# Performance work log

Measured on AMD Instinct MI355X. Metric: run time of the kernel, lower is better.

Reference implementation:

```python
import jax, jax.numpy as jnp
import numpy as np

PAD, BOS, EOS = 0, 1, 2
VOCAB, EMB, HID, BATCH, MAXLEN = 32, 64, 1024, 2048, 100


def setup_inputs() -> dict:
    key = jax.random.key(0)
    ks = jax.random.split(key, 11)
    s = 0.08  # small init scale keeps softmax/sigmoid in a sane range
    g = lambda k, shape: (s * jax.random.normal(k, shape)).astype(jnp.float32)
    emb = g(ks[0], (VOCAB, EMB)).at[PAD].set(0.0)  # padding_idx row = 0
    return {
        "prevs": jnp.full((BATCH, 1), BOS, dtype=jnp.int32),
        "emb": emb,
        "Wih0": g(ks[1], (4 * HID, EMB)),
        "Whh0": g(ks[2], (4 * HID, HID)),
        "bih0": g(ks[3], (4 * HID,)),
        "bhh0": g(ks[4], (4 * HID,)),
        "Wih1": g(ks[5], (4 * HID, HID)),
        "Whh1": g(ks[6], (4 * HID, HID)),
        "bih1": g(ks[7], (4 * HID,)),
        "bhh1": g(ks[8], (4 * HID,)),
        "Wout": g(ks[9], (VOCAB, HID)),
        "bout": g(ks[10], (VOCAB,)),
        "max_len": MAXLEN,
    }


def _lstm_cell(x, h, c, Wih, Whh, bih, bhh):
    # torch LSTM gate order: i, f, g, o
    gates = x @ Wih.T + bih + h @ Whh.T + bhh  # [n, 4H]
    i, f, g, o = jnp.split(gates, 4, axis=-1)
    c = jax.nn.sigmoid(f) * c + jax.nn.sigmoid(i) * jnp.tanh(g)
    h = jax.nn.sigmoid(o) * jnp.tanh(c)
    return h, c


def reference(prevs, emb, Wih0, Whh0, bih0, bhh0, Wih1, Whh1, bih1, bhh1,
              Wout, bout, max_len):
    n = prevs.shape[0]
    H = Whh0.shape[1]
    prev = prevs[:, 0].astype(jnp.int32)
    h0 = jnp.zeros((n, H), jnp.float32)
    c0 = jnp.zeros((n, H), jnp.float32)
    h1 = jnp.zeros((n, H), jnp.float32)
    c1 = jnp.zeros((n, H), jnp.float32)
    is_end = prev == EOS
    lengths = jnp.zeros((n,), jnp.int32)
    keys = jax.random.split(jax.random.key(42), max_len)

    def step(carry, k):
        prev, h0, c0, h1, c1, is_end, lengths = carry
        x = emb[prev]                                   # [n, E]
        h0, c0 = _lstm_cell(x, h0, c0, Wih0, Whh0, bih0, bhh0)
        h1, c1 = _lstm_cell(h0, h1, c1, Wih1, Whh1, bih1, bhh1)
        logits = h1 @ Wout.T + bout                     # [n, V]
        cur = jax.random.categorical(k, logits).astype(jnp.int32)
        cur = jnp.where(is_end, PAD, cur)               # finished rows emit PAD
        lengths = lengths + (~is_end).astype(jnp.int32)
        is_end = is_end | (cur == EOS)
        return (cur, h0, c0, h1, c1, is_end, lengths), cur

    carry, seq = jax.lax.scan(step, (prev, h0, c0, h1, c1, is_end, lengths), keys)
    lengths = carry[6] + 1                               # +1 for BOS, as in sample_tensor
    sequences = jnp.concatenate([prevs.astype(jnp.int32), seq.T], axis=1)  # [n, 1+max_len]
    return sequences, lengths
```

## Files before the change

kernel.cpp:

```cpp
#include <hip/hip_runtime.h>
#include <cstdint>
#include <cstddef>


constexpr int PAD_TOK = 0, BOS_TOK = 1, EOS_TOK = 2;
constexpr int VOCAB = 32, EMB = 64, HID = 1024, BATCH = 2048, MAXLEN = 100;
constexpr int BK = 32;
constexpr int NKT_H = HID / BK;
constexpr float SCALE = 64.0f;
constexpr double INV_S2 = 1.0 / 4096.0;

using half8 = __attribute__((ext_vector_type(8))) _Float16;
using f32x4 = __attribute__((ext_vector_type(4))) float;
typedef unsigned short u16;
typedef uint32_t u32;

__device__ __forceinline__ u32 rotl32(u32 v, int d) {
  return (v << d) | (v >> (32 - d));
}

__device__ __forceinline__ void threefry2x32(u32 k0, u32 k1, u32 x0, u32 x1,
                                             u32& y0, u32& y1) {
  const u32 k2 = k0 ^ k1 ^ 0x1BD11BDAu;
#define TF_ROUND(r) do { x0 += x1; x1 = rotl32(x1, (r)); x1 ^= x0; } while (0)
  x0 += k0; x1 += k1;
  TF_ROUND(13); TF_ROUND(15); TF_ROUND(26); TF_ROUND(6);
  x0 += k1; x1 += k2 + 1u;
  TF_ROUND(17); TF_ROUND(29); TF_ROUND(16); TF_ROUND(24);
  x0 += k2; x1 += k0 + 2u;
  TF_ROUND(13); TF_ROUND(15); TF_ROUND(26); TF_ROUND(6);
  x0 += k0; x1 += k1 + 3u;
  TF_ROUND(17); TF_ROUND(29); TF_ROUND(16); TF_ROUND(24);
  x0 += k1; x1 += k2 + 4u;
  TF_ROUND(13); TF_ROUND(15); TF_ROUND(26); TF_ROUND(6);
  x0 += k2; x1 += k0 + 5u;
#undef TF_ROUND
  y0 = x0; y1 = x1;
}

__device__ __forceinline__ void gl_lds16(const void* g, void* l) {
  __builtin_amdgcn_global_load_lds(
      (const __attribute__((address_space(1))) void*)g,
      (__attribute__((address_space(3))) void*)l, 16, 0, 0);
}

__device__ __forceinline__ double rcp1p(double q) {
  const double d = 1.0 + q;
  double r = (double)__builtin_amdgcn_rcpf((float)d);
  r = r * fma(-d, r, 2.0);
  r = r * fma(-d, r, 2.0);
  return r;
}
__device__ __forceinline__ double exp2d(double t) {
  const double n = rint(t);
  const double f = t - n;
  double p = 1.0178086009239699e-07;
  p = fma(p, f, 1.3215542443841225e-06);
  p = fma(p, f, 1.5252733804059840e-05);
  p = fma(p, f, 1.5403530393381610e-04);
  p = fma(p, f, 1.3333558146428443e-03);
  p = fma(p, f, 9.6181291076284772e-03);
  p = fma(p, f, 5.5504108664821580e-02);
  p = fma(p, f, 2.4022650695910071e-01);
  p = fma(p, f, 6.9314718055994531e-01);
  p = fma(p, f, 1.0);
  const long long e = ((long long)(int)n + 1023) << 52;
  return p * __longlong_as_double(e);
}
__device__ __forceinline__ double sigd(double x) {
  return rcp1p(exp2d(x * -1.4426950408889634));
}
__device__ __forceinline__ double tanhd(double x) {
  return fma(2.0, rcp1p(exp2d(x * -2.8853900817779268)), -1.0);
}

__global__ __launch_bounds__(256) void pack_w(
    const float* __restrict__ src, int K, int nkt,
    uint4* __restrict__ dhi, uint4* __restrict__ dlo, int nchunks) {
  const int g = blockIdx.x * 256 + threadIdx.x;
  if (g >= nchunks) return;
  const int ut = g / (nkt * 512);
  const int rem = g - ut * (nkt * 512);
  const int kt = rem >> 9;
  const int slot = rem & 511;
  const int fm = slot >> 6, kg = (slot >> 4) & 3, r15 = slot & 15;
  const int row = (fm & 3) * HID + ut * 32 + (fm >> 2) * 16 + r15;
  const int col = kt * 32 + kg * 8;
  const float* s = src + (size_t)row * K + col;
  u16 hh[8], ll[8];
#pragma unroll
  for (int e = 0; e < 8; ++e) {
    const float x = s[e] * SCALE;
    const _Float16 h = (_Float16)x;
    const float rm = x - (float)h;
    const _Float16 l = (_Float16)rm;
    hh[e] = __builtin_bit_cast(u16, h);
    ll[e] = __builtin_bit_cast(u16, l);
  }
  dhi[g] = make_uint4((u32)hh[0] | ((u32)hh[1] << 16),
                      (u32)hh[2] | ((u32)hh[3] << 16),
                      (u32)hh[4] | ((u32)hh[5] << 16),
                      (u32)hh[6] | ((u32)hh[7] << 16));
  dlo[g] = make_uint4((u32)ll[0] | ((u32)ll[1] << 16),
                      (u32)ll[2] | ((u32)ll[3] << 16),
                      (u32)ll[4] | ((u32)ll[5] << 16),
                      (u32)ll[6] | ((u32)ll[7] << 16));
}

__global__ __launch_bounds__(256) void split_kernel(
    const float* __restrict__ src, u16* __restrict__ hi, u16* __restrict__ lo,
    int n) {
  const int i = blockIdx.x * 256 + threadIdx.x;
  if (i >= n) return;
  const float x = src[i] * SCALE;
  const _Float16 h = (_Float16)x;
  const float rem = x - (float)h;
  const _Float16 l = (_Float16)rem;
  hi[i] = __builtin_bit_cast(u16, h);
  lo[i] = __builtin_bit_cast(u16, l);
}

__global__ __launch_bounds__(256) void init_kernel(
    const int* __restrict__ prevs, float* __restrict__ c0,
    float* __restrict__ c1, u16* __restrict__ h0hi0, u16* __restrict__ h0lo0,
    u16* __restrict__ h0hi1, u16* __restrict__ h0lo1,
    u16* __restrict__ h1hi0, u16* __restrict__ h1lo0,
    u16* __restrict__ h1hi1, u16* __restrict__ h1lo1,
    int* __restrict__ prev, int* __restrict__ is_end,
    int* __restrict__ lengths, u32* __restrict__ keys,
    int* __restrict__ out_tok) {
  const int tid = blockIdx.x * 256 + threadIdx.x;
  const int total = BATCH * HID;
  if (tid < total) {
    c0[tid] = 0.0f; c1[tid] = 0.0f;
    h0hi0[tid] = 0; h0lo0[tid] = 0; h0hi1[tid] = 0; h0lo1[tid] = 0;
    h1hi0[tid] = 0; h1lo0[tid] = 0; h1hi1[tid] = 0; h1lo1[tid] = 0;
  }
  if (tid < BATCH) {
    const int p = prevs[tid];
    prev[tid] = p;
    is_end[tid] = (p == EOS_TOK) ? 1 : 0;
    lengths[tid] = 0;
    out_tok[(size_t)tid * (MAXLEN + 1)] = p;
  }
  if (tid < MAXLEN) {
    u32 y0, y1;
    threefry2x32(0u, 42u, 0u, (u32)tid, y0, y1);
    keys[2 * tid] = y0;
    keys[2 * tid + 1] = y1;
  }
}

template <bool GATHER, bool WRITE_F32>
__global__ __launch_bounds__(512) void lstm_mfma(
    const uint4* __restrict__ A0p_hi, const uint4* __restrict__ A0p_lo,
    const u16* __restrict__ Ehi, const u16* __restrict__ Elo,
    const int* __restrict__ ptok, int nk0,
    const uint4* __restrict__ A1p_hi, const uint4* __restrict__ A1p_lo,
    const uint4* __restrict__ W0hi, const uint4* __restrict__ W0lo,
    const uint4* __restrict__ W1hi, const uint4* __restrict__ W1lo,
    const float* __restrict__ bih, const float* __restrict__ bhh,
    float* __restrict__ Cst, float* __restrict__ Hf32,
    uint4* __restrict__ Hp_hi, uint4* __restrict__ Hp_lo) {
  __shared__ uint4 lds4[6144];
  char* lds = (char*)lds4;

  const int tid = threadIdx.x;
  const int lane = tid & 63;
  const int wid = tid >> 6;
  const int wm = wid >> 1, wn = wid & 1;

  const int bid = blockIdx.x;
  const int swz = (bid & 7) * 32 + (bid >> 3);
  const int ut = swz >> 3;
  const int mt = swz & 7;
  const int u0 = ut * 32;
  const int row0 = mt * 256;

  const int r15 = lane & 15;
  const int kgrp = lane >> 4;
  int tok[2];
  if (GATHER) {
#pragma unroll
    for (int j = 0; j < 2; ++j)
      tok[j] = ptok[row0 + (j * 8 + wid) * 16 + r15];
  }

  const int NT = nk0 + NKT_H;

  auto ldsA = [&](int buf, int pl, int slot) -> char* {
    return lds + buf * 49152 + pl * 16384 + slot * 16;
  };
  auto ldsW = [&](int buf, int pl, int slot) -> char* {
    return lds + buf * 49152 + 32768 + pl * 8192 + slot * 16;
  };

  auto stage = [&](int buf, int kt) {
    const bool s0 = kt < nk0;
    const int ktl = s0 ? kt : kt - nk0;
    const uint4* wh = s0 ? W0hi : W1hi;
    const uint4* wl = s0 ? W0lo : W1lo;
    const int wbase = (ut * (s0 ? nk0 : NKT_H) + ktl) * 512;
    {
      const int sb = wid * 64;
      gl_lds16(wh + wbase + sb + lane, ldsW(buf, 0, sb));
      gl_lds16(wl + wbase + sb + lane, ldsW(buf, 1, sb));
    }
    if (GATHER && s0) {
#pragma unroll
      for (int j = 0; j < 2; ++j) {
        const int sb = j * 512 + wid * 64;
        const size_t ao = (size_t)tok[j] * EMB + ktl * 32 + kgrp * 8;
        gl_lds16(Ehi + ao, ldsA(buf, 0, sb));
        gl_lds16(Elo + ao, ldsA(buf, 1, sb));
      }
    } else {
      const uint4* ah_ = s0 ? A0p_hi : A1p_hi;
      const uint4* al_ = s0 ? A0p_lo : A1p_lo;
      const int abase = (mt * NKT_H + ktl) * 1024;
#pragma unroll
      for (int j = 0; j < 2; ++j) {
        const int sb = j * 512 + wid * 64;
        gl_lds16(ah_ + abase + sb + lane, ldsA(buf, 0, sb));
        gl_lds16(al_ + abase + sb + lane, ldsA(buf, 1, sb));
      }
    }
  };

  f32x4 acc[4][4] = {};

  auto compute = [&](int buf) {
    half8 ah[4], al[4];
#pragma unroll
    for (int mi = 0; mi < 4; ++mi) {
      ah[mi] = *(const half8*)ldsA(buf, 0, (wm * 4 + mi) * 64 + lane);
      al[mi] = *(const half8*)ldsA(buf, 1, (wm * 4 + mi) * 64 + lane);
    }
#pragma unroll
    for (int ni = 0; ni < 4; ++ni) {
      const half8 bh = *(const half8*)ldsW(buf, 0, (wn * 4 + ni) * 64 + lane);
      const half8 bl = *(const half8*)ldsW(buf, 1, (wn * 4 + ni) * 64 + lane);
#pragma unroll
      for (int mi = 0; mi < 4; ++mi) {
        acc[mi][ni] =
            __builtin_amdgcn_mfma_f32_16x16x32_f16(ah[mi], bh, acc[mi][ni], 0, 0, 0);
        acc[mi][ni] =
            __builtin_amdgcn_mfma_f32_16x16x32_f16(ah[mi], bl, acc[mi][ni], 0, 0, 0);
        acc[mi][ni] =
            __builtin_amdgcn_mfma_f32_16x16x32_f16(al[mi], bh, acc[mi][ni], 0, 0, 0);
      }
    }
  };

  stage(0, 0);
  __syncthreads();
#pragma unroll 1
  for (int t = 0; t < NT; ++t) {
    if (t + 1 < NT) stage((t + 1) & 1, t + 1);
    compute(t & 1);
    __syncthreads();
  }

  const int u_loc = wn * 16 + r15;
  const int u = u0 + u_loc;
  double bsum[4];
#pragma unroll
  for (int g = 0; g < 4; ++g)
    bsum[g] = (double)bih[g * HID + u] + (double)bhh[g * HID + u];

  float* Cb = Cst + (size_t)(mt * 32 + ut) * 8192;
  u16* hhT = (u16*)lds;
  u16* hlT = (u16*)(lds + 20480);
  const int hi4 = lane >> 4;

#pragma unroll
  for (int mi = 0; mi < 4; ++mi) {
#pragma unroll
    for (int r = 0; r < 4; ++r) {
      const int row = wm * 64 + mi * 16 + hi4 * 4 + r;
      const double gI = (double)acc[mi][0][r] * INV_S2 + bsum[0];
      const double gF = (double)acc[mi][1][r] * INV_S2 + bsum[1];
      const double gG = (double)acc[mi][2][r] * INV_S2 + bsum[2];
      const double gO = (double)acc[mi][3][r] * INV_S2 + bsum[3];
      const double ii = sigd(gI);
      const double ff = sigd(gF);
      const double gt = tanhd(gG);
      const double oo = sigd(gO);
      const int co = row * 32 + u_loc;
      const double cn = ff * (double)Cb[co] + ii * gt;
      Cb[co] = (float)cn;
      const float hf = (float)(oo * tanhd(cn));
      if (WRITE_F32) Hf32[(size_t)(row0 + row) * HID + u] = hf;
      const float hs = hf * SCALE;
      const _Float16 hh = (_Float16)hs;
      const float rm = hs - (float)hh;
      const _Float16 hl = (_Float16)rm;
      hhT[row * 40 + u_loc] = __builtin_bit_cast(u16, hh);
      hlT[row * 40 + u_loc] = __builtin_bit_cast(u16, hl);
    }
  }
  __syncthreads();

  const size_t mtut = ((size_t)mt * NKT_H + ut) * 1024;
#pragma unroll
  for (int j = 0; j < 2; ++j) {
    const int g = tid + j * 512;
    const int fA = g >> 6, kg = (g >> 4) & 3, rr = g & 15;
    const int row = fA * 16 + rr;
    const uint4 vh = *(const uint4*)(hhT + row * 40 + kg * 8);
    const uint4 vl = *(const uint4*)(hlT + row * 40 + kg * 8);
    Hp_hi[mtut + g] = vh;
    Hp_lo[mtut + g] = vl;
  }
}

__global__ __launch_bounds__(256) void sample_kernel(
    const float* __restrict__ h1, const float* __restrict__ Wout,
    const float* __restrict__ bout, const u32* __restrict__ keys, int t,
    int* __restrict__ prev, int* __restrict__ is_end, int* __restrict__ lengths,
    int* __restrict__ out_tok, int* __restrict__ len_out) {
  const int wave = threadIdx.x >> 6;
  const int lane = threadIdx.x & 63;
  const int row = blockIdx.x * 4 + wave;
  const int v = lane & 31;
  const int half = lane >> 5;

  const float* hseg = h1 + (size_t)row * HID + half * (HID / 2);
  const float* wseg = Wout + (size_t)v * HID + half * (HID / 2);

  double acc = 0.0;
#pragma unroll 4
  for (int k = 0; k < HID / 2; k += 4) {
    const float4 w = *(const float4*)(wseg + k);
    const float4 h = *(const float4*)(hseg + k);
    acc = fma((double)w.x, (double)h.x, acc);
    acc = fma((double)w.y, (double)h.y, acc);
    acc = fma((double)w.z, (double)h.z, acc);
    acc = fma((double)w.w, (double)h.w, acc);
  }
  acc += __shfl_xor(acc, 32);

  const u32 k0 = keys[2 * t], k1 = keys[2 * t + 1];
  u32 y0, y1;
  threefry2x32(k0, k1, 0u, (u32)(row * VOCAB + v), y0, y1);
  const u32 bits = y0 ^ y1;
  const float f = __uint_as_float((bits >> 9) | 0x3f800000u) - 1.0f;
  const float uu = fmaxf(f, 1.17549435e-38f);
  const double g = -log(-log((double)uu));

  double z = acc + (double)bout[v] + g;
  int idx = v;
#pragma unroll
  for (int m = 1; m < 32; m <<= 1) {
    const double zo = __shfl_xor(z, m);
    const int io = __shfl_xor(idx, m);
    if (zo > z || (zo == z && io < idx)) { z = zo; idx = io; }
  }

  if (lane == 0) {
    const int e = is_end[row];
    const int cur = e ? PAD_TOK : idx;
    const int len = lengths[row] + (e ? 0 : 1);
    const int enew = e | (cur == EOS_TOK ? 1 : 0);
    prev[row] = cur;
    is_end[row] = enew;
    lengths[row] = len;
    out_tok[(size_t)row * (MAXLEN + 1) + t + 1] = cur;
    if (len_out) len_out[row] = len + 1;
  }
}

extern "C" void kernel_launch(void* const* d_in, const int* in_sizes, int n_in,
                              void* d_out, int out_size, void* d_ws,
                              size_t ws_size, hipStream_t stream) {
  const int* prevs = (const int*)d_in[0];
  const float* emb = (const float*)d_in[1];
  const float* Wih0 = (const float*)d_in[2];
  const float* Whh0 = (const float*)d_in[3];
  const float* bih0 = (const float*)d_in[4];
  const float* bhh0 = (const float*)d_in[5];
  const float* Wih1 = (const float*)d_in[6];
  const float* Whh1 = (const float*)d_in[7];
  const float* bih1 = (const float*)d_in[8];
  const float* bhh1 = (const float*)d_in[9];
  const float* Wout = (const float*)d_in[10];
  const float* bout = (const float*)d_in[11];

  const size_t SH = (size_t)BATCH * HID;
  const size_t CH = SH / 8;
  const size_t CW = (size_t)32 * NKT_H * 512;
  const size_t CW0 = (size_t)32 * 2 * 512;

  float* c0 = (float*)d_ws;
  float* c1 = c0 + SH;
  float* h1f = c1 + SH;
  uint4* q = (uint4*)(h1f + SH);
  uint4* ph0hi[2] = {q, q + CH};
  uint4* ph0lo[2] = {q + 2 * CH, q + 3 * CH};
  uint4* ph1hi[2] = {q + 4 * CH, q + 5 * CH};
  uint4* ph1lo[2] = {q + 6 * CH, q + 7 * CH};
  uint4* pw = q + 8 * CH;
  uint4* pwih0h = pw;              uint4* pwih0l = pwih0h + CW0;
  uint4* pwhh0h = pwih0l + CW0;    uint4* pwhh0l = pwhh0h + CW;
  uint4* pwih1h = pwhh0l + CW;     uint4* pwih1l = pwih1h + CW;
  uint4* pwhh1h = pwih1l + CW;     uint4* pwhh1l = pwhh1h + CW;
  u16* embh = (u16*)(pwhh1l + CW);
  u16* embl = embh + VOCAB * EMB;
  int* prev = (int*)(embl + VOCAB * EMB);
  int* is_end = prev + BATCH;
  int* lengths = is_end + BATCH;
  u32* keys = (u32*)(lengths + BATCH);

  int* out_tok = (int*)d_out;
  int* len_out = out_tok + (size_t)BATCH * (MAXLEN + 1);

  init_kernel<<<dim3((BATCH * HID) / 256), 256, 0, stream>>>(
      prevs, c0, c1, (u16*)ph0hi[0], (u16*)ph0lo[0], (u16*)ph0hi[1],
      (u16*)ph0lo[1], (u16*)ph1hi[0], (u16*)ph1lo[0], (u16*)ph1hi[1],
      (u16*)ph1lo[1], prev, is_end, lengths, keys, out_tok);

  split_kernel<<<dim3((VOCAB * EMB + 255) / 256), 256, 0, stream>>>(
      emb, embh, embl, VOCAB * EMB);
  pack_w<<<dim3((int)((CW0 + 255) / 256)), 256, 0, stream>>>(
      Wih0, EMB, 2, pwih0h, pwih0l, (int)CW0);
  pack_w<<<dim3((int)((CW + 255) / 256)), 256, 0, stream>>>(
      Whh0, HID, NKT_H, pwhh0h, pwhh0l, (int)CW);
  pack_w<<<dim3((int)((CW + 255) / 256)), 256, 0, stream>>>(
      Wih1, HID, NKT_H, pwih1h, pwih1l, (int)CW);
  pack_w<<<dim3((int)((CW + 255) / 256)), 256, 0, stream>>>(
      Whh1, HID, NKT_H, pwhh1h, pwhh1l, (int)CW);

  int p = 0;
  for (int t = 0; t < MAXLEN; ++t) {
    lstm_mfma<true, false><<<dim3(256), 512, 0, stream>>>(
        nullptr, nullptr, embh, embl, prev, 2, ph0hi[p], ph0lo[p],
        pwih0h, pwih0l, pwhh0h, pwhh0l, bih0, bhh0, c0, nullptr,
        ph0hi[p ^ 1], ph0lo[p ^ 1]);
    lstm_mfma<false, true><<<dim3(256), 512, 0, stream>>>(
        ph0hi[p ^ 1], ph0lo[p ^ 1], nullptr, nullptr, nullptr, NKT_H,
        ph1hi[p], ph1lo[p], pwih1h, pwih1l, pwhh1h, pwhh1l, bih1, bhh1,
        c1, h1f, ph1hi[p ^ 1], ph1lo[p ^ 1]);
    sample_kernel<<<dim3(BATCH / 4), 256, 0, stream>>>(
        h1f, Wout, bout, keys, t, prev, is_end, lengths, out_tok,
        (t == MAXLEN - 1) ? len_out : nullptr);
    p ^= 1;
  }
  (void)in_sizes; (void)n_in; (void)out_size; (void)ws_size;
}
```

Baseline: 17.63 ms.

## Load A operands directly into registers and shrink LDS for two blocks per CU

```diff
diff --git a/kernel.cpp b/kernel.cpp
--- a/kernel.cpp
+++ b/kernel.cpp
@@ -152,7 +152,7 @@
 }
 
 template <bool GATHER, bool WRITE_F32>
-__global__ __launch_bounds__(512) void lstm_mfma(
+__global__ __launch_bounds__(512, 2) void lstm_mfma(
     const uint4* __restrict__ A0p_hi, const uint4* __restrict__ A0p_lo,
     const u16* __restrict__ Ehi, const u16* __restrict__ Elo,
     const int* __restrict__ ptok, int nk0,
@@ -162,7 +162,7 @@
     const float* __restrict__ bih, const float* __restrict__ bhh,
     float* __restrict__ Cst, float* __restrict__ Hf32,
     uint4* __restrict__ Hp_hi, uint4* __restrict__ Hp_lo) {
-  __shared__ uint4 lds4[6144];
+  __shared__ uint4 lds4[2560];
   char* lds = (char*)lds4;
 
   const int tid = threadIdx.x;
@@ -179,62 +179,60 @@
 
   const int r15 = lane & 15;
   const int kgrp = lane >> 4;
-  int tok[2];
+
+  int tok4[4];
   if (GATHER) {
 #pragma unroll
-    for (int j = 0; j < 2; ++j)
-      tok[j] = ptok[row0 + (j * 8 + wid) * 16 + r15];
+    for (int mi = 0; mi < 4; ++mi)
+      tok4[mi] = ptok[row0 + (wm * 4 + mi) * 16 + r15];
   }
 
   const int NT = nk0 + NKT_H;
 
-  auto ldsA = [&](int buf, int pl, int slot) -> char* {
-    return lds + buf * 49152 + pl * 16384 + slot * 16;
+  auto ldsW = [&](int buf, int pl, int slot) -> char* {
+    return lds + buf * 16384 + pl * 8192 + slot * 16;
   };
-  auto ldsW = [&](int buf, int pl, int slot) -> char* {
-    return lds + buf * 49152 + 32768 + pl * 8192 + slot * 16;
-  };
-
-  auto stage = [&](int buf, int kt) {
+
+  auto stageW = [&](int buf, int kt) {
     const bool s0 = kt < nk0;
     const int ktl = s0 ? kt : kt - nk0;
     const uint4* wh = s0 ? W0hi : W1hi;
     const uint4* wl = s0 ? W0lo : W1lo;
-    const int wbase = (ut * (s0 ? nk0 : NKT_H) + ktl) * 512;
-    {
-      const int sb = wid * 64;
-      gl_lds16(wh + wbase + sb + lane, ldsW(buf, 0, sb));
-      gl_lds16(wl + wbase + sb + lane, ldsW(buf, 1, sb));
-    }
+    const int wbase = (ut * (s0 ? nk0 : NKT_H) + ktl) * 512 + wid * 64;
+    gl_lds16(wh + wbase + lane, ldsW(buf, 0, wid * 64));
+    gl_lds16(wl + wbase + lane, ldsW(buf, 1, wid * 64));
+  };
+
+  auto loadA = [&](int kt, uint4* Ah, uint4* Al) {
+    const bool s0 = kt < nk0;
+    const int ktl = s0 ? kt : kt - nk0;
     if (GATHER && s0) {
 #pragma unroll
-      for (int j = 0; j < 2; ++j) {
-        const int sb = j * 512 + wid * 64;
-        const size_t ao = (size_t)tok[j] * EMB + ktl * 32 + kgrp * 8;
-        gl_lds16(Ehi + ao, ldsA(buf, 0, sb));
-        gl_lds16(Elo + ao, ldsA(buf, 1, sb));
+      for (int mi = 0; mi < 4; ++mi) {
+        const size_t ao = (size_t)tok4[mi] * EMB + ktl * 32 + kgrp * 8;
+        Ah[mi] = *(const uint4*)(Ehi + ao);
+        Al[mi] = *(const uint4*)(Elo + ao);
       }
     } else {
       const uint4* ah_ = s0 ? A0p_hi : A1p_hi;
       const uint4* al_ = s0 ? A0p_lo : A1p_lo;
-      const int abase = (mt * NKT_H + ktl) * 1024;
-#pragma unroll
-      for (int j = 0; j < 2; ++j) {
-        const int sb = j * 512 + wid * 64;
-        gl_lds16(ah_ + abase + sb + lane, ldsA(buf, 0, sb));
-        gl_lds16(al_ + abase + sb + lane, ldsA(buf, 1, sb));
+      const int ab = (mt * NKT_H + ktl) * 1024 + wm * 256 + lane;
+#pragma unroll
+      for (int mi = 0; mi < 4; ++mi) {
+        Ah[mi] = ah_[ab + mi * 64];
+        Al[mi] = al_[ab + mi * 64];
       }
     }
   };
 
   f32x4 acc[4][4] = {};
 
-  auto compute = [&](int buf) {
+  auto compute = [&](const uint4* AhF, const uint4* AlF, int buf) {
     half8 ah[4], al[4];
 #pragma unroll
     for (int mi = 0; mi < 4; ++mi) {
-      ah[mi] = *(const half8*)ldsA(buf, 0, (wm * 4 + mi) * 64 + lane);
-      al[mi] = *(const half8*)ldsA(buf, 1, (wm * 4 + mi) * 64 + lane);
+      ah[mi] = __builtin_bit_cast(half8, AhF[mi]);
+      al[mi] = __builtin_bit_cast(half8, AlF[mi]);
     }
 #pragma unroll
     for (int ni = 0; ni < 4; ++ni) {
@@ -252,12 +250,21 @@
     }
   };
 
-  stage(0, 0);
+  uint4 Ah0[4], Al0[4], Ah1[4], Al1[4];
+  loadA(0, Ah0, Al0);
+  stageW(0, 0);
   __syncthreads();
 #pragma unroll 1
-  for (int t = 0; t < NT; ++t) {
-    if (t + 1 < NT) stage((t + 1) & 1, t + 1);
-    compute(t & 1);
+  for (int t = 0; t < NT; t += 2) {
+    loadA(t + 1, Ah1, Al1);
+    stageW(1, t + 1);
+    compute(Ah0, Al0, 0);
+    __syncthreads();
+    if (t + 2 < NT) {
+      loadA(t + 2, Ah0, Al0);
+      stageW(0, t + 2);
+    }
+    compute(Ah1, Al1, 1);
     __syncthreads();
   }
 
```

Result: slower. 18.63 ms (+5.7%).
